# Performance work log

Measured on AMD Instinct MI355X. Metric: run time of the kernel, lower is better.

Reference implementation:

```python
import jax, jax.numpy as jnp
import numpy as np

B, S, D, H, FFN = 2, 2048, 1024, 8, 4096
DK = D // H            # head key/query dim = 128
VD = 2 * D             # double_v_dim -> v_dim = 2048
DV = VD // H           # per-head value dim = 256
SCALE_BASE = 512.0
EPS = 1e-5


def _dup_interleave(m):
    # (S, d/2) -> (S, d), each column repeated twice adjacently
    return jnp.repeat(m, 2, axis=-1)


def _rotate_every_two(x):
    x1 = x[..., 0::2]
    x2 = x[..., 1::2]
    return jnp.stack((-x2, x1), axis=-1).reshape(x.shape)


def _xpos(x, downscale):
    # x: (B,H,S,d) -- XPOS rotary with length-dependent scale
    d = x.shape[-1]
    pos = jnp.arange(x.shape[-2], dtype=jnp.float32)
    sv = (jnp.arange(0, d, 2, dtype=jnp.float32) + 0.4 * d) / (1.4 * d)  # (d/2,)
    scale = sv[None, :] ** (pos / SCALE_BASE)[:, None]                    # (S, d/2)
    half = d // 2
    inv_freq = 1.0 / (10000.0 ** (jnp.arange(half, dtype=jnp.float32) / half))
    sinusoid = pos[:, None] * inv_freq[None, :]                           # (S, d/2)
    if downscale:
        scale = 1.0 / scale
    sin = _dup_interleave(jnp.sin(sinusoid) * scale)                      # (S, d)
    cos = _dup_interleave(jnp.cos(sinusoid) * scale)
    return x * cos + _rotate_every_two(x) * sin


def _gammas(heads):
    return 1.0 - jnp.exp(jnp.linspace(np.log(1 / 32), np.log(1 / 512), heads)).astype(jnp.float32)


def _layernorm(x, w, b):
    mu = jnp.mean(x, axis=-1, keepdims=True)
    var = jnp.var(x, axis=-1, keepdims=True)
    return (x - mu) * jax.lax.rsqrt(var + EPS) * w + b


def setup_inputs() -> dict:
    key = jax.random.key(0)
    ks = jax.random.split(key, 16)
    sD = 1.0 / np.sqrt(D)
    sF = 1.0 / np.sqrt(FFN)
    return {
        "X": jax.random.normal(ks[0], (B, S, D), jnp.float32),
        "Wq": jax.random.normal(ks[1], (H, D, DK), jnp.float32) * sD,
        "Wk": jax.random.normal(ks[2], (H, D, DK), jnp.float32) * sD,
        "Wv": jax.random.normal(ks[3], (H, D, DV), jnp.float32) * sD,
        "W_G": jax.random.normal(ks[4], (D, VD), jnp.float32) * sD,
        "W_O": jax.random.normal(ks[5], (VD, D), jnp.float32) / np.sqrt(VD),
        "gn_w": jnp.ones((VD,), jnp.float32),
        "gn_b": jnp.zeros((VD,), jnp.float32),
        "ln1_w": jnp.ones((D,), jnp.float32),
        "ln1_b": jnp.zeros((D,), jnp.float32),
        "ln2_w": jnp.ones((D,), jnp.float32),
        "ln2_b": jnp.zeros((D,), jnp.float32),
        "ffn_w1": jax.random.normal(ks[6], (D, FFN), jnp.float32) * sD,
        "ffn_b1": jnp.zeros((FFN,), jnp.float32),
        "ffn_w2": jax.random.normal(ks[7], (FFN, D), jnp.float32) * sF,
        "ffn_b2": jnp.zeros((D,), jnp.float32),
    }


def _retention(Xn, Wq, Wk, Wv, W_G, W_O, gn_w, gn_b):
    # Xn: (B,S,D) pre-normalized input
    Q = jnp.einsum("bsd,hdk->bhsk", Xn, Wq)
    K = jnp.einsum("bsd,hdk->bhsk", Xn, Wk)
    V = jnp.einsum("bsd,hdv->bhsv", Xn, Wv)
    Q = _xpos(Q, downscale=False)
    K = _xpos(K, downscale=True)
    # decay matrix D[h,n,m] = gamma_h^(n-m) for n>=m else 0
    n = jnp.arange(S)[:, None]
    m = jnp.arange(S)[None, :]
    mask = (n >= m)
    exponent = jnp.where(mask, (n - m).astype(jnp.float32), 0.0)
    g = _gammas(H)
    Dmat = jnp.where(mask[None], g[:, None, None] ** exponent[None], 0.0)  # (H,S,S)
    ret = jnp.einsum("bhsk,bhtk->bhst", Q, K) * Dmat[None]
    Y = jnp.einsum("bhst,bhtv->bhsv", ret, V)                              # (B,H,S,DV)
    Y = jnp.transpose(Y, (0, 2, 1, 3))                                     # (B,S,H,DV)
    # GroupNorm(heads, v_dim) applied per token: normalize within each head chunk
    mu = jnp.mean(Y, axis=-1, keepdims=True)
    var = jnp.var(Y, axis=-1, keepdims=True)
    Y = (Y - mu) * jax.lax.rsqrt(var + EPS)
    Y = Y.reshape(B, S, VD) * gn_w + gn_b
    G = Xn @ W_G
    gated = (G * jax.nn.sigmoid(G)) * Y                                     # swish gate
    return gated @ W_O


def reference(X, Wq, Wk, Wv, W_G, W_O, gn_w, gn_b, ln1_w, ln1_b, ln2_w, ln2_b,
              ffn_w1, ffn_b1, ffn_w2, ffn_b2):
    X = _retention(_layernorm(X, ln1_w, ln1_b), Wq, Wk, Wv, W_G, W_O, gn_w, gn_b) + X
    h = _layernorm(X, ln2_w, ln2_b)
    h = jax.nn.gelu(h @ ffn_w1 + ffn_b1, approximate=False) @ ffn_w2 + ffn_b2
    return h + X
```

## Files before the change

kernel.cpp:

```cpp
#include <hip/hip_runtime.h>
#include <hip/hip_bf16.h>

typedef unsigned short u16;
typedef unsigned int   u32;
typedef short short8 __attribute__((ext_vector_type(8)));
typedef float f32x4  __attribute__((ext_vector_type(4)));

__device__ __forceinline__ float b2f(u16 u) { return __uint_as_float(((u32)u) << 16); }
__device__ __forceinline__ u16 f2b(float f) {
    u32 u = __float_as_uint(f);
    u += 0x7FFF + ((u >> 16) & 1);
    return (u16)(u >> 16);
}
__device__ __forceinline__ float gelu_fast(float v) {
    float a = v * (2.302118f + 0.102953f * v * v);
    a = fminf(a, 120.f);
    float e = exp2f(a);
    return v * e / (1.f + e);
}

typedef const unsigned int __attribute__((address_space(1)))* gas1;
typedef unsigned int __attribute__((address_space(3)))* las3;
__device__ __forceinline__ void async_ld16(const void* g, const void* l) {
    __builtin_amdgcn_global_load_lds((gas1)(unsigned long long)g,
                                     (las3)(unsigned int)(unsigned long long)l,
                                     16, 0, 0);
}

__device__ __forceinline__ void wtrans_body(const float* __restrict__ W, u16* __restrict__ Wt,
                                            int K, int N, int bx, int by, int bz) {
    __shared__ u16 tile[32][36];
    const int k0 = bx * 32, n0 = by * 32;
    const float* Wz = W + (long)bz * K * N;
    u16* Wtz = Wt + (long)bz * K * N;
    const int t = threadIdx.x;
    const int r = t >> 3, c = (t & 7) * 4;
    float4 v = *(const float4*)(Wz + (long)(k0 + r) * N + n0 + c);
    tile[r][c+0] = f2b(v.x); tile[r][c+1] = f2b(v.y);
    tile[r][c+2] = f2b(v.z); tile[r][c+3] = f2b(v.w);
    __syncthreads();
    uint2 pk;
    pk.x = (u32)tile[c+0][r] | ((u32)tile[c+1][r] << 16);
    pk.y = (u32)tile[c+2][r] | ((u32)tile[c+3][r] << 16);
    *(uint2*)(Wtz + (long)(n0 + r) * K + k0 + c) = pk;
}

__device__ __forceinline__ void xtab_body(float4* __restrict__ tab, int blk) {
    int idx = blk * 256 + threadIdx.x;
    int j = idx & 63, s = idx >> 6;
    float sv = (2.f * j + 51.2f) / 179.2f;
    float scale = exp2f(log2f(sv) * ((float)s * (1.f / 512.f)));
    float inv_freq = exp2f((float)j * (-13.287712379549449f / 64.f));
    float ang = (float)s * inv_freq;
    float sn = sinf(ang), cs = cosf(ang);
    tab[idx] = make_float4(cs * scale, sn * scale, cs / scale, sn / scale);
}

__device__ __forceinline__ void ln_body(const float* __restrict__ X,
                                        const float* __restrict__ w,
                                        const float* __restrict__ bb,
                                        u16* __restrict__ out, long row) {
    const int t = threadIdx.x;
    float4 p = ((const float4*)(X + row * 1024))[t];
    float x[4] = { p.x, p.y, p.z, p.w };
    float s = x[0]+x[1]+x[2]+x[3];
    float q = x[0]*x[0]+x[1]*x[1]+x[2]*x[2]+x[3]*x[3];
#pragma unroll
    for (int o = 32; o > 0; o >>= 1) { s += __shfl_down(s, o, 64); q += __shfl_down(q, o, 64); }
    __shared__ float aS[4], aQ[4];
    if ((t & 63) == 0) { aS[t >> 6] = s; aQ[t >> 6] = q; }
    __syncthreads();
    s = aS[0]+aS[1]+aS[2]+aS[3];
    q = aQ[0]+aQ[1]+aQ[2]+aQ[3];
    float mean = s * (1.f/1024.f);
    float var  = q * (1.f/1024.f) - mean*mean;
    float rstd = rsqrtf(var + 1e-5f);
    float4 wv = ((const float4*)w)[t];
    float4 bv = ((const float4*)bb)[t];
    uint2 r;
    r.x = (u32)f2b((x[0]-mean)*rstd*wv.x + bv.x) | ((u32)f2b((x[1]-mean)*rstd*wv.y + bv.y) << 16);
    r.y = (u32)f2b((x[2]-mean)*rstd*wv.z + bv.z) | ((u32)f2b((x[3]-mean)*rstd*wv.w + bv.w) << 16);
    ((uint2*)(out + row * 1024))[t] = r;
}

__global__ __launch_bounds__(256) void prep_k(
    const float* __restrict__ Wq, const float* __restrict__ Wk,
    const float* __restrict__ Wv, const float* __restrict__ WG,
    const float* __restrict__ WO, const float* __restrict__ fw1,
    const float* __restrict__ fw2, const float* __restrict__ X,
    const float* __restrict__ ln1w, const float* __restrict__ ln1b,
    u16* __restrict__ WT, u16* __restrict__ WOT,
    u16* __restrict__ fw1T, u16* __restrict__ fw2T,
    float4* __restrict__ xtab, u16* __restrict__ Xn) {
    const int id = blockIdx.x;
    if (id < 16384) {
        const float* W; u16* Wt; int K, N, bx, by, bz = 0;
        if (id < 1024)       { W=Wq;  Wt=WT;           K=1024; N=128;  int l=id;       bx=l&31;  by=(l>>5)&3; bz=l>>7; }
        else if (id < 2048)  { W=Wk;  Wt=WT+1048576;   K=1024; N=128;  int l=id-1024;  bx=l&31;  by=(l>>5)&3; bz=l>>7; }
        else if (id < 4096)  { W=Wv;  Wt=WT+2097152;   K=1024; N=256;  int l=id-2048;  bx=l&31;  by=(l>>5)&7; bz=l>>8; }
        else if (id < 6144)  { W=WG;  Wt=WT+4194304;   K=1024; N=2048; int l=id-4096;  bx=l&31;  by=l>>5; }
        else if (id < 8192)  { W=WO;  Wt=WOT;          K=2048; N=1024; int l=id-6144;  bx=l&63;  by=l>>6; }
        else if (id < 12288) { W=fw1; Wt=fw1T;         K=1024; N=4096; int l=id-8192;  bx=l&31;  by=l>>5; }
        else                 { W=fw2; Wt=fw2T;         K=4096; N=1024; int l=id-12288; bx=l&127; by=l>>7; }
        wtrans_body(W, Wt, K, N, bx, by, bz);
    } else if (id < 16896) {
        xtab_body(xtab, id - 16384);
    } else {
        ln_body(X, ln1w, ln1b, Xn, id - 16896);
    }
}

__global__ __launch_bounds__(256) void ln2_combine(const float* __restrict__ P,
                                                   const float* __restrict__ X,
                                                   const float* __restrict__ w,
                                                   const float* __restrict__ bb,
                                                   float* __restrict__ X2,
                                                   u16* __restrict__ hb) {
    const long row = blockIdx.x;
    const int t = threadIdx.x;
    const float* p = P + row * 3072;
    float4 a = ((const float4*)p)[t];
    float4 c = ((const float4*)(p + 1024))[t];
    float4 xr = ((const float4*)(X + row * 1024))[t];
    float x[4] = { a.x+c.x+xr.x, a.y+c.y+xr.y, a.z+c.z+xr.z, a.w+c.w+xr.w };
    ((float4*)(X2 + row * 1024))[t] = make_float4(x[0], x[1], x[2], x[3]);
    float s = x[0]+x[1]+x[2]+x[3];
    float q = x[0]*x[0]+x[1]*x[1]+x[2]*x[2]+x[3]*x[3];
#pragma unroll
    for (int o = 32; o > 0; o >>= 1) { s += __shfl_down(s, o, 64); q += __shfl_down(q, o, 64); }
    __shared__ float aS[4], aQ[4];
    if ((t & 63) == 0) { aS[t >> 6] = s; aQ[t >> 6] = q; }
    __syncthreads();
    s = aS[0]+aS[1]+aS[2]+aS[3];
    q = aQ[0]+aQ[1]+aQ[2]+aQ[3];
    float mean = s * (1.f/1024.f);
    float var  = q * (1.f/1024.f) - mean*mean;
    float rstd = rsqrtf(var + 1e-5f);
    float4 wv = ((const float4*)w)[t];
    float4 bv = ((const float4*)bb)[t];
    uint2 r;
    r.x = (u32)f2b((x[0]-mean)*rstd*wv.x + bv.x) | ((u32)f2b((x[1]-mean)*rstd*wv.y + bv.y) << 16);
    r.y = (u32)f2b((x[2]-mean)*rstd*wv.z + bv.z) | ((u32)f2b((x[3]-mean)*rstd*wv.w + bv.w) << 16);
    ((uint2*)(hb + row * 1024))[t] = r;
}

__global__ __launch_bounds__(256) void ffn2_combine(const float* __restrict__ P,
                                                    const float* __restrict__ b2,
                                                    const float* __restrict__ X2,
                                                    float* __restrict__ out) {
    const long row = blockIdx.x;
    const int t = threadIdx.x;
    float4 p0 = ((const float4*)(P + row * 1024))[t];
    float4 p1 = ((const float4*)(P + 16777216 + row * 1024))[t];
    float4 x2 = ((const float4*)(X2 + row * 1024))[t];
    float4 bv = ((const float4*)b2)[t];
    ((float4*)(out + row * 1024))[t] = make_float4(
        p0.x + p1.x + x2.x + bv.x, p0.y + p1.y + x2.y + bv.y,
        p0.z + p1.z + x2.z + bv.z, p0.w + p1.w + x2.w + bv.w);
}

enum { EPI_GELU_BIAS = 2, EPI_QKVG = 4 };

template<int EPI, int PANELS>
__global__ __launch_bounds__(256) void mgemm(
    const u16* __restrict__ A, const u16* __restrict__ Bt, u16* __restrict__ Cv,
    int K, int aStride, long cStride,
    const float* __restrict__ bias, u16* __restrict__ Vt) {
    __shared__ __align__(16) u16 As[PANELS * 4096];
    __shared__ __align__(16) u16 Bs[PANELS * 4096];
    const int pid = blockIdx.x;
    const int mb = pid & 31;
    const int nb = pid >> 5;
    const int t = threadIdx.x;
    const int row0 = mb * 128, col0 = nb * 128;
    const int wave = t >> 6, lane = t & 63;
    const int wm = wave >> 1, wn = wave & 1;
    const int quad = lane >> 4, l16 = lane & 15;
    const int sgc = ((t & 3) ^ ((t >> 3) & 3)) * 8;
    const u16* Ag = A + (long)(row0 + (t >> 2)) * aStride + sgc;
    const u16* Bg = Bt + (long)(col0 + (t >> 2)) * K + sgc;
    const long aj = (long)64 * aStride;
    const long bj = (long)64 * K;
    const u32 lo = __builtin_amdgcn_readfirstlane((u32)(wave * 1024));
    const int swr = ((l16 >> 1) & 3) << 3;

    f32x4 acc[4][4];
#pragma unroll
    for (int i = 0; i < 4; i++)
#pragma unroll
        for (int j = 0; j < 4; j++) acc[i][j] = (f32x4){0.f, 0.f, 0.f, 0.f};

    for (int k0 = 0; k0 < K; k0 += PANELS * 32) {
#pragma unroll
        for (int h = 0; h < PANELS; h++) {
            const u16* Agh = Ag + k0 + h * 32;
            const u16* Bgh = Bg + k0 + h * 32;
            async_ld16(Agh,      (const char*)As + h*8192 + lo);
            async_ld16(Agh + aj, (const char*)As + h*8192 + 4096 + lo);
            async_ld16(Bgh,      (const char*)Bs + h*8192 + lo);
            async_ld16(Bgh + bj, (const char*)Bs + h*8192 + 4096 + lo);
        }
        __syncthreads();
#pragma unroll
        for (int h = 0; h < PANELS; h++) {
            short8 af[4], bf[4];
#pragma unroll
            for (int mt = 0; mt < 4; mt++)
                af[mt] = *(const short8*)(As + h*4096 + (wm*64 + mt*16 + l16) * 32 + ((quad*8) ^ swr));
#pragma unroll
            for (int nt = 0; nt < 4; nt++)
                bf[nt] = *(const short8*)(Bs + h*4096 + (wn*64 + nt*16 + l16) * 32 + ((quad*8) ^ swr));
#pragma unroll
            for (int mt = 0; mt < 4; mt++)
#pragma unroll
                for (int nt = 0; nt < 4; nt++)
                    acc[mt][nt] = __builtin_amdgcn_mfma_f32_16x16x32_bf16(af[mt], bf[nt], acc[mt][nt], 0, 0, 0);
        }
        __syncthreads();
    }

    if constexpr (EPI == EPI_QKVG) {
        if (col0 >= 2048 && col0 < 4096) {
            const int bq = row0 >> 11;
            const int sb = (row0 & 2047) + wm*64 + quad*4;
#pragma unroll
            for (int mt = 0; mt < 4; mt++) {
#pragma unroll
                for (int nt = 0; nt < 4; nt++) {
                    int vc = (col0 - 2048) + wn*64 + nt*16 + l16;
                    u16* dst = Vt + ((long)((bq << 3) + (vc >> 8)) * 256 + (vc & 255)) * 2048
                                  + sb + mt*16;
                    uint2 pk;
                    pk.x = (u32)f2b(acc[mt][nt][0]) | ((u32)f2b(acc[mt][nt][1]) << 16);
                    pk.y = (u32)f2b(acc[mt][nt][2]) | ((u32)f2b(acc[mt][nt][3]) << 16);
                    *(uint2*)dst = pk;
                }
            }
            return;
        }
    }

#pragma unroll
    for (int mt = 0; mt < 4; mt++) {
#pragma unroll
        for (int reg = 0; reg < 4; reg++) {
            int r = row0 + wm*64 + mt*16 + quad*4 + reg;
#pragma unroll
            for (int nt = 0; nt < 4; nt++) {
                int c = col0 + wn*64 + nt*16 + l16;
                float v = acc[mt][nt][reg];
                if constexpr (EPI == EPI_GELU_BIAS) {
                    v = gelu_fast(v + bias[c]);
                } else if constexpr (EPI == EPI_QKVG) {
                    if (c < 2048) {
                        int j = (c & 127) >> 1;
                        float4 tb = ((const float4*)bias)[((r & 2047) << 6) + j];
                        float cs = (c < 1024) ? tb.x : tb.z;
                        float sn = (c < 1024) ? tb.y : tb.w;
                        float partner = __shfl_xor(v, 1, 64);
                        v = v * cs + ((c & 1) ? partner : -partner) * sn;
                    }
                }
                Cv[(long)r * cStride + c] = f2b(v);
            }
        }
    }
}

__global__ __launch_bounds__(256) void mgemm_sk(
    const u16* __restrict__ A, const u16* __restrict__ Bt, float* __restrict__ P,
    int K, int kHalf, int aStride, long pRowStride, long sliceOff) {
    __shared__ __align__(16) u16 As[4 * 4096];
    __shared__ __align__(16) u16 Bs[4 * 4096];
    const int pid = blockIdx.x;
    const int mb = pid & 31;
    const int nb = (pid & 255) >> 5;
    const int slice = pid >> 8;
    const int t = threadIdx.x;
    const int row0 = mb * 128, col0 = nb * 128;
    const int wave = t >> 6, lane = t & 63;
    const int wm = wave >> 1, wn = wave & 1;
    const int quad = lane >> 4, l16 = lane & 15;
    const int sgc = ((t & 3) ^ ((t >> 3) & 3)) * 8;
    const u16* Ag = A + (long)(row0 + (t >> 2)) * aStride + sgc;
    const u16* Bg = Bt + (long)(col0 + (t >> 2)) * K + sgc;
    const long aj = (long)64 * aStride;
    const long bj = (long)64 * K;
    const u32 lo = __builtin_amdgcn_readfirstlane((u32)(wave * 1024));
    const int swr = ((l16 >> 1) & 3) << 3;

    f32x4 acc[4][4];
#pragma unroll
    for (int i = 0; i < 4; i++)
#pragma unroll
        for (int j = 0; j < 4; j++) acc[i][j] = (f32x4){0.f, 0.f, 0.f, 0.f};

    const int kBeg = slice * kHalf;
    const int nsteps = kHalf >> 6;

    auto stage = [&](int k0, int bb) {
#pragma unroll
        for (int h = 0; h < 2; h++) {
            const u16* Agh = Ag + k0 + h * 32;
            const u16* Bgh = Bg + k0 + h * 32;
            async_ld16(Agh,      (const char*)As + bb*16384 + h*8192 + lo);
            async_ld16(Agh + aj, (const char*)As + bb*16384 + h*8192 + 4096 + lo);
            async_ld16(Bgh,      (const char*)Bs + bb*16384 + h*8192 + lo);
            async_ld16(Bgh + bj, (const char*)Bs + bb*16384 + h*8192 + 4096 + lo);
        }
    };

    stage(kBeg, 0);
    for (int i = 0; i < nsteps; i++) {
        const int buf = i & 1;
        if (i + 1 < nsteps) {
            stage(kBeg + (i + 1) * 64, buf ^ 1);
            asm volatile("s_waitcnt vmcnt(8)" ::: "memory");
        } else {
            asm volatile("s_waitcnt vmcnt(0)" ::: "memory");
        }
        __builtin_amdgcn_s_barrier();
#pragma unroll
        for (int h = 0; h < 2; h++) {
            short8 af[4], bf[4];
#pragma unroll
            for (int mt = 0; mt < 4; mt++)
                af[mt] = *(const short8*)(As + buf*8192 + h*4096 + (wm*64 + mt*16 + l16) * 32 + ((quad*8) ^ swr));
#pragma unroll
            for (int nt = 0; nt < 4; nt++)
                bf[nt] = *(const short8*)(Bs + buf*8192 + h*4096 + (wn*64 + nt*16 + l16) * 32 + ((quad*8) ^ swr));
#pragma unroll
            for (int mt = 0; mt < 4; mt++)
#pragma unroll
                for (int nt = 0; nt < 4; nt++)
                    acc[mt][nt] = __builtin_amdgcn_mfma_f32_16x16x32_bf16(af[mt], bf[nt], acc[mt][nt], 0, 0, 0);
        }
        __builtin_amdgcn_s_barrier();
    }

    float* Pb = P + slice * sliceOff;
#pragma unroll
    for (int mt = 0; mt < 4; mt++) {
#pragma unroll
        for (int reg = 0; reg < 4; reg++) {
            int r = row0 + wm*64 + mt*16 + quad*4 + reg;
#pragma unroll
            for (int nt = 0; nt < 4; nt++) {
                int c = col0 + wn*64 + nt*16 + l16;
                Pb[(long)r * pRowStride + c] = acc[mt][nt][reg];
            }
        }
    }
}

__global__ __launch_bounds__(256) void retention_mfma(
    u16* __restrict__ QKVG, const u16* __restrict__ Vt,
    const float* __restrict__ gnw, const float* __restrict__ gnb) {
    __shared__ __align__(16) u16 Qs[4][64][32];
    __shared__ __align__(16) u16 Ks[2][4][32][32];
    __shared__ __align__(16) u16 Vs[2][256][32];
    __shared__ u16 Ss[64][40];
    const int id = blockIdx.x;
    const int halfg = id >> 8, r5 = id & 255;
    const int bh = r5 >> 4, i16 = r5 & 15;
    const int tile = halfg ? i16 : 31 - i16;
    const int b = bh >> 3, h = bh & 7;
    const int t = threadIdx.x;
    const int wave = t >> 6, lane = t & 63, quad = lane >> 4, l16 = lane & 15;
    const u32 lo = __builtin_amdgcn_readfirstlane((u32)(wave * 1024));
    const u16* Qbase = QKVG + (long)b * 2048 * 6144 + h * 128;
    const u16* Kbase = Qbase + 1024;
    const u16* Vbase = Vt + (long)(b * 8 + h) * 256 * 2048;
    u16* Gseg = QKVG + (long)b * 2048 * 6144 + 4096 + h * 256;
    const int sq8 = (((l16 & 3) ^ ((l16 >> 2) & 3))) << 3;

    float g = 1.f - expf(-3.4657359027997265f + (-0.3960841031771116f) * (float)h);
    float log2g = log2f(g);
    const float gi16 = exp2f(log2g * -16.f);
    const float gi32 = gi16 * gi16;
    const float gf[4] = {1.f, g, g*g, g*g*g};
    const int srow0 = tile*64 + wave*16 + quad*4;
    float drun = exp2f(log2g * (float)(srow0 - l16));

    auto issueKV = [&](int jt, int buf) {
#pragma unroll
        for (int i = 0; i < 2; i++) {
            int c = t + i * 256;
            int ks = c >> 7, row = (c >> 2) & 31;
            int cbs = (c & 3) ^ ((c >> 2) & 3) ^ ((c >> 4) & 3);
            async_ld16(Kbase + (long)(jt*32 + row) * 6144 + ks*32 + cbs*8,
                       (const char*)Ks + buf*8192 + i*4096 + lo);
        }
#pragma unroll
        for (int i = 0; i < 4; i++) {
            int c = t + i * 256;
            int row = c >> 2;
            int cbs = (c & 3) ^ ((c >> 2) & 3) ^ ((c >> 4) & 3);
            async_ld16(Vbase + (long)row * 2048 + jt*32 + cbs*8,
                       (const char*)Vs + buf*16384 + i*4096 + lo);
        }
    };

#pragma unroll
    for (int i = 0; i < 4; i++) {
        int c = t + i * 256;
        int ks = c >> 8, row = (c >> 2) & 63;
        int cbs = (c & 3) ^ ((c >> 2) & 3) ^ ((c >> 4) & 3);
        async_ld16(Qbase + (long)(tile*64 + row) * 6144 + ks*32 + cbs*8,
                   (const char*)Qs + i*4096 + lo);
    }
    issueKV(0, 0);

    float gw[16], gbv[16];
#pragma unroll
    for (int nt = 0; nt < 16; nt++) {
        gw[nt]  = gnw[h*256 + nt*16 + l16];
        gbv[nt] = gnb[h*256 + nt*16 + l16];
    }
    f32x4 oacc[16];
#pragma unroll
    for (int nt = 0; nt < 16; nt++) oacc[nt] = (f32x4){0.f, 0.f, 0.f, 0.f};
    __syncthreads();

    const int njt = 2 * tile + 2;
    for (int jt = 0; jt < njt; jt++) {
        const int cur = jt & 1;
        if (jt + 1 < njt) issueKV(jt + 1, cur ^ 1);
        f32x4 s0 = (f32x4){0.f,0.f,0.f,0.f}, s1 = (f32x4){0.f,0.f,0.f,0.f};
#pragma unroll
        for (int ks = 0; ks < 4; ks++) {
            short8 aq = *(const short8*)&Qs[ks][wave*16 + l16][(quad*8) ^ sq8];
            short8 b0 = *(const short8*)&Ks[cur][ks][l16][(quad*8) ^ sq8];
            short8 b1 = *(const short8*)&Ks[cur][ks][16 + l16][(quad*8) ^ sq8];
            s0 = __builtin_amdgcn_mfma_f32_16x16x32_bf16(aq, b0, s0, 0, 0, 0);
            s1 = __builtin_amdgcn_mfma_f32_16x16x32_bf16(aq, b1, s1, 0, 0, 0);
        }
#pragma unroll
        for (int reg = 0; reg < 4; reg++) {
            int srow = srow0 + reg;
            int tc0 = jt*32 + l16, tc1 = tc0 + 16;
            float dbase = drun * gf[reg];
            float d0 = (srow >= tc0) ? dbase : 0.f;
            float d1 = (srow >= tc1) ? dbase * gi16 : 0.f;
            Ss[wave*16 + quad*4 + reg][l16]      = f2b(s0[reg] * d0);
            Ss[wave*16 + quad*4 + reg][16 + l16] = f2b(s1[reg] * d1);
        }
        drun *= gi32;
        short8 as = *(const short8*)&Ss[wave*16 + l16][quad*8];
#pragma unroll
        for (int nt = 0; nt < 16; nt++) {
            short8 bv = *(const short8*)&Vs[cur][nt*16 + l16][(quad*8) ^ sq8];
            oacc[nt] = __builtin_amdgcn_mfma_f32_16x16x32_bf16(as, bv, oacc[nt], 0, 0, 0);
        }
        __syncthreads();
    }

#pragma unroll
    for (int reg = 0; reg < 4; reg++) {
        float s = 0.f, q = 0.f;
#pragma unroll
        for (int nt = 0; nt < 16; nt++) { float v = oacc[nt][reg]; s += v; q += v*v; }
#pragma unroll
        for (int m = 1; m < 16; m <<= 1) { s += __shfl_xor(s, m, 16); q += __shfl_xor(q, m, 16); }
        float mean = s * (1.f/256.f);
        float var  = q * (1.f/256.f) - mean*mean;
        float rstd = rsqrtf(var + 1e-5f);
        int srow = srow0 + reg;
        u16* grow = Gseg + (long)srow * 6144;
#pragma unroll
        for (int nt = 0; nt < 16; nt++) {
            float gval = b2f(grow[nt*16 + l16]);
            float y = (oacc[nt][reg] - mean) * rstd * gw[nt] + gbv[nt];
            float sg = gval / (1.f + exp2f(-1.4426950408889634f * gval));
            grow[nt*16 + l16] = f2b(sg * y);
        }
    }
}

extern "C" void kernel_launch(void* const* d_in, const int* in_sizes, int n_in,
                              void* d_out, int out_size, void* d_ws, size_t ws_size,
                              hipStream_t stream) {
    (void)in_sizes; (void)n_in; (void)out_size; (void)ws_size;
    const float* X    = (const float*)d_in[0];
    const float* Wq   = (const float*)d_in[1];
    const float* Wk   = (const float*)d_in[2];
    const float* Wv   = (const float*)d_in[3];
    const float* WG   = (const float*)d_in[4];
    const float* WO   = (const float*)d_in[5];
    const float* gnw  = (const float*)d_in[6];
    const float* gnb  = (const float*)d_in[7];
    const float* ln1w = (const float*)d_in[8];
    const float* ln1b = (const float*)d_in[9];
    const float* ln2w = (const float*)d_in[10];
    const float* ln2b = (const float*)d_in[11];
    const float* fw1  = (const float*)d_in[12];
    const float* fb1  = (const float*)d_in[13];
    const float* fw2  = (const float*)d_in[14];
    const float* fb2  = (const float*)d_in[15];

    constexpr int D = 1024, FFN = 4096;
    constexpr int M = 4096;
    constexpr long MB = 1048576;

    char* ws = (char*)d_ws;
    u16* WT   = (u16*)(ws + 0*MB);
    u16* WOT  = (u16*)(ws + 12*MB);
    u16* fw1T = (u16*)(ws + 16*MB);
    u16* fw2T = (u16*)(ws + 24*MB);
    u16*   QKVG = (u16*)(ws + 32*MB);
    u16*   Xn   = (u16*)(ws + 80*MB);
    float4* xtab= (float4*)(ws + 88*MB);
    u16*   Vt   = (u16*)(ws + 90*MB);
    float* X2   = (float*)(ws + 80*MB);
    u16*   hb   = (u16*)(ws + 0*MB);
    u16*   mid  = (u16*)(ws + 32*MB);
    float* PF   = (float*)(ws + 0*MB);

    prep_k<<<20992, 256, 0, stream>>>(Wq, Wk, Wv, WG, WO, fw1, fw2, X, ln1w, ln1b,
                                      WT, WOT, fw1T, fw2T, xtab, Xn);
    mgemm<EPI_QKVG, 1><<<1536, 256, 0, stream>>>(
        Xn, WT, QKVG, D, D, 6144, (const float*)xtab, Vt);
    retention_mfma<<<512, 256, 0, stream>>>(QKVG, Vt, gnw, gnb);
    mgemm_sk<<<512, 256, 0, stream>>>(
        QKVG + 4096, WOT, (float*)QKVG, 2048, 1024, 6144, 3072, 1024);
    ln2_combine<<<M, 256, 0, stream>>>((const float*)QKVG, X, ln2w, ln2b, X2, hb);
    mgemm<EPI_GELU_BIAS, 2><<<1024, 256, 0, stream>>>(
        hb, fw1T, mid, D, D, FFN, fb1, nullptr);
    mgemm_sk<<<512, 256, 0, stream>>>(
        mid, fw2T, PF, 4096, 2048, 4096, 1024, 16777216);
    ffn2_combine<<<M, 256, 0, stream>>>(PF, fb2, X2, (float*)d_out);
}
```

Baseline: 432.8 us.

## Double-buffer LDS tiles in mgemm with async prefetch of next K slice

Result: faster. 412.7 us (-4.6%).

```diff
diff --git a/kernel.cpp b/kernel.cpp
--- a/kernel.cpp
+++ b/kernel.cpp
@@ -161,13 +161,13 @@
 
 enum { EPI_GELU_BIAS = 2, EPI_QKVG = 4 };
 
-template<int EPI, int PANELS>
+template<int EPI>
 __global__ __launch_bounds__(256) void mgemm(
     const u16* __restrict__ A, const u16* __restrict__ Bt, u16* __restrict__ Cv,
     int K, int aStride, long cStride,
     const float* __restrict__ bias, u16* __restrict__ Vt) {
-    __shared__ __align__(16) u16 As[PANELS * 4096];
-    __shared__ __align__(16) u16 Bs[PANELS * 4096];
+    __shared__ __align__(16) u16 As[2 * 4096];
+    __shared__ __align__(16) u16 Bs[2 * 4096];
     const int pid = blockIdx.x;
     const int mb = pid & 31;
     const int nb = pid >> 5;
@@ -190,33 +190,39 @@
 #pragma unroll
         for (int j = 0; j < 4; j++) acc[i][j] = (f32x4){0.f, 0.f, 0.f, 0.f};
 
-    for (int k0 = 0; k0 < K; k0 += PANELS * 32) {
-#pragma unroll
-        for (int h = 0; h < PANELS; h++) {
-            const u16* Agh = Ag + k0 + h * 32;
-            const u16* Bgh = Bg + k0 + h * 32;
-            async_ld16(Agh,      (const char*)As + h*8192 + lo);
-            async_ld16(Agh + aj, (const char*)As + h*8192 + 4096 + lo);
-            async_ld16(Bgh,      (const char*)Bs + h*8192 + lo);
-            async_ld16(Bgh + bj, (const char*)Bs + h*8192 + 4096 + lo);
-        }
-        __syncthreads();
-#pragma unroll
-        for (int h = 0; h < PANELS; h++) {
-            short8 af[4], bf[4];
-#pragma unroll
-            for (int mt = 0; mt < 4; mt++)
-                af[mt] = *(const short8*)(As + h*4096 + (wm*64 + mt*16 + l16) * 32 + ((quad*8) ^ swr));
+    auto stage = [&](int k0, int bb) {
+        const u16* Agh = Ag + k0;
+        const u16* Bgh = Bg + k0;
+        async_ld16(Agh,      (const char*)As + bb*8192 + lo);
+        async_ld16(Agh + aj, (const char*)As + bb*8192 + 4096 + lo);
+        async_ld16(Bgh,      (const char*)Bs + bb*8192 + lo);
+        async_ld16(Bgh + bj, (const char*)Bs + bb*8192 + 4096 + lo);
+    };
+
+    const int nT = K >> 5;
+    stage(0, 0);
+    for (int i = 0; i < nT; i++) {
+        const int buf = i & 1;
+        if (i + 1 < nT) {
+            stage((i + 1) * 32, buf ^ 1);
+            asm volatile("s_waitcnt vmcnt(4)" ::: "memory");
+        } else {
+            asm volatile("s_waitcnt vmcnt(0)" ::: "memory");
+        }
+        __builtin_amdgcn_s_barrier();
+        short8 af[4], bf[4];
+#pragma unroll
+        for (int mt = 0; mt < 4; mt++)
+            af[mt] = *(const short8*)(As + buf*4096 + (wm*64 + mt*16 + l16) * 32 + ((quad*8) ^ swr));
+#pragma unroll
+        for (int nt = 0; nt < 4; nt++)
+            bf[nt] = *(const short8*)(Bs + buf*4096 + (wn*64 + nt*16 + l16) * 32 + ((quad*8) ^ swr));
+#pragma unroll
+        for (int mt = 0; mt < 4; mt++)
 #pragma unroll
             for (int nt = 0; nt < 4; nt++)
-                bf[nt] = *(const short8*)(Bs + h*4096 + (wn*64 + nt*16 + l16) * 32 + ((quad*8) ^ swr));
-#pragma unroll
-            for (int mt = 0; mt < 4; mt++)
-#pragma unroll
-                for (int nt = 0; nt < 4; nt++)
-                    acc[mt][nt] = __builtin_amdgcn_mfma_f32_16x16x32_bf16(af[mt], bf[nt], acc[mt][nt], 0, 0, 0);
-        }
-        __syncthreads();
+                acc[mt][nt] = __builtin_amdgcn_mfma_f32_16x16x32_bf16(af[mt], bf[nt], acc[mt][nt], 0, 0, 0);
+        __builtin_amdgcn_s_barrier();
     }
 
     if constexpr (EPI == EPI_QKVG) {
@@ -518,13 +524,13 @@
 
     prep_k<<<20992, 256, 0, stream>>>(Wq, Wk, Wv, WG, WO, fw1, fw2, X, ln1w, ln1b,
                                       WT, WOT, fw1T, fw2T, xtab, Xn);
-    mgemm<EPI_QKVG, 1><<<1536, 256, 0, stream>>>(
+    mgemm<EPI_QKVG><<<1536, 256, 0, stream>>>(
         Xn, WT, QKVG, D, D, 6144, (const float*)xtab, Vt);
     retention_mfma<<<512, 256, 0, stream>>>(QKVG, Vt, gnw, gnb);
     mgemm_sk<<<512, 256, 0, stream>>>(
         QKVG + 4096, WOT, (float*)QKVG, 2048, 1024, 6144, 3072, 1024);
     ln2_combine<<<M, 256, 0, stream>>>((const float*)QKVG, X, ln2w, ln2b, X2, hb);
-    mgemm<EPI_GELU_BIAS, 2><<<1024, 256, 0, stream>>>(
+    mgemm<EPI_GELU_BIAS><<<1024, 256, 0, stream>>>(
         hb, fw1T, mid, D, D, FFN, fb1, nullptr);
     mgemm_sk<<<512, 256, 0, stream>>>(
         mid, fw2T, PF, 4096, 2048, 4096, 1024, 16777216);
```
